# Kernel optimization log

Measured on AMD Instinct MI355X. Metric: run time of the kernel, lower is better.

The kernel has to match this reference:

```python
import jax, jax.numpy as jnp
import numpy as np

B, N, D_IN, D_OUT = 4, 2048, 1024, 1024

def setup_inputs() -> dict:
    key = jax.random.key(0)
    ks = jax.random.split(key, 7)
    s_in = 1.0 / np.sqrt(D_IN)
    return {
        "X": jax.random.normal(ks[0], (B, N, D_IN), dtype=jnp.float32),
        "Wq": jax.random.uniform(ks[1], (D_IN, D_OUT), jnp.float32, -s_in, s_in),
        "bq": jax.random.uniform(ks[2], (D_OUT,), jnp.float32, -s_in, s_in),
        "Wk": jax.random.uniform(ks[3], (D_IN, D_OUT), jnp.float32, -s_in, s_in),
        "bk": jax.random.uniform(ks[4], (D_OUT,), jnp.float32, -s_in, s_in),
        "Wv": jax.random.uniform(ks[5], (D_IN, D_OUT), jnp.float32, -s_in, s_in),
        "bv": jax.random.uniform(ks[6], (D_OUT,), jnp.float32, -s_in, s_in),
    }

def reference(X, Wq, bq, Wk, bk, Wv, bv):
    # QKV projections: [B,N,D_in] @ [D_in,D_out] -> [B,N,D_out]
    q = jnp.einsum('bnd,de->bne', X, Wq) + bq
    k = jnp.einsum('bnd,de->bne', X, Wk) + bk
    v = jnp.einsum('bnd,de->bne', X, Wv) + bv
    # Unscaled attention (faithful: original has no 1/sqrt(d))
    scores = jnp.einsum('bne,bme->bnm', q, k)  # [B,N,N]
    weights = jax.nn.softmax(scores, axis=-1)
    return jnp.einsum('bnm,bme->bne', weights, v)
```

## Files before the change

### kernel.cpp

```cpp
#include <hip/hip_runtime.h>
#include <hip/hip_bf16.h>
#include <hip/hip_fp16.h>
#include <stdint.h>
#include <math.h>


typedef unsigned short ushort_t;
typedef __attribute__((ext_vector_type(8))) _Float16  f16x8;
typedef __attribute__((ext_vector_type(4))) _Float16  f16x4;
typedef __attribute__((ext_vector_type(4))) float     f32x4;

__device__ __forceinline__ void async_load16(const void* g, void* l) {
  __builtin_amdgcn_global_load_lds(
      (const __attribute__((address_space(1))) void*)g,
      (__attribute__((address_space(3))) void*)l, 16, 0, 0);
}

__global__ __launch_bounds__(256)
void zv_gemm_kernel(const ushort_t* __restrict__ A, const ushort_t* __restrict__ BT,
                    const float* __restrict__ wkbq, const float* __restrict__ bvp,
                    __half* __restrict__ Zh, ushort_t* __restrict__ Vt)
{
  const int K = 1024;
  __shared__ ushort_t As[2][128 * 32];
  __shared__ ushort_t Bs[2][128 * 32];

  const int t    = threadIdx.x;
  const int lane = t & 63;
  const int wave = t >> 6;
  const int wm   = (wave >> 1) * 64;
  const int wn   = (wave & 1) * 64;

  const ushort_t* Ab = A + (long)blockIdx.y * 128 * K;
  const ushort_t* Bb = BT + (long)blockIdx.x * 128 * K;

  const int ldr = t >> 2;
  const int swzs = (ldr & 3) ^ ((ldr >> 2) & 3);
  const int ldc = ((t & 3) ^ swzs) * 8;
  const int frow = lane & 15;
  const int fsz  = (frow & 3) ^ ((frow >> 2) & 3);
  const int fo   = (((lane >> 4) ^ fsz)) * 8;

  f32x4 acc[4][4];
  const f32x4 zero = {0.0f, 0.0f, 0.0f, 0.0f};
#pragma unroll
  for (int i = 0; i < 4; ++i)
#pragma unroll
    for (int j = 0; j < 4; ++j) acc[i][j] = zero;

  for (int k0 = 0; k0 < K; k0 += 64) {
    __syncthreads();
    const ushort_t* ga = Ab + (long)ldr * K + k0 + ldc;
    const ushort_t* gb = Bb + (long)ldr * K + k0 + ldc;
#pragma unroll
    for (int h = 0; h < 2; ++h) {
      async_load16(ga + h * 32,                &As[h][t * 8]);
      async_load16(ga + h * 32 + 64 * (long)K, &As[h][2048 + t * 8]);
      async_load16(gb + h * 32,                &Bs[h][t * 8]);
      async_load16(gb + h * 32 + 64 * (long)K, &Bs[h][2048 + t * 8]);
    }
    __syncthreads();
#pragma unroll
    for (int h = 0; h < 2; ++h) {
      f16x8 af[4], bf[4];
#pragma unroll
      for (int i = 0; i < 4; ++i) {
        af[i] = *(const f16x8*)&As[h][(wm + i * 16 + frow) * 32 + fo];
        bf[i] = *(const f16x8*)&Bs[h][(wn + i * 16 + frow) * 32 + fo];
      }
#pragma unroll
      for (int mi = 0; mi < 4; ++mi)
#pragma unroll
        for (int ni = 0; ni < 4; ++ni)
          acc[mi][ni] = __builtin_amdgcn_mfma_f32_16x16x32_f16(af[mi], bf[ni], acc[mi][ni], 0, 0, 0);
    }
  }

  const int er = (lane >> 4) * 4;
  const int ec = lane & 15;
  const int tgt = blockIdx.x >> 3;
#pragma unroll
  for (int ni = 0; ni < 4; ++ni) {
    const int c = (blockIdx.x & 7) * 128 + wn + ni * 16 + ec;
    const float bval = (tgt == 0) ? wkbq[c] : bvp[c];
#pragma unroll
    for (int mi = 0; mi < 4; ++mi) {
      const long grow0 = (long)blockIdx.y * 128 + wm + mi * 16 + er;
      if (tgt == 0) {
#pragma unroll
        for (int r = 0; r < 4; ++r)
          Zh[(grow0 + r) * 1024 + c] = __float2half(acc[mi][ni][r] + bval);
      } else {
        const long b  = grow0 >> 11;
        const long ml = grow0 & 2047;
        f16x4 v4;
#pragma unroll
        for (int r = 0; r < 4; ++r) v4[r] = (_Float16)(acc[mi][ni][r] + bval);
        *(f16x4*)&Vt[b * 2097152 + (long)c * 2048 + ml] = v4;
      }
    }
  }
}

__global__ __launch_bounds__(256)
void gemm_f16_kernel(const ushort_t* __restrict__ A, const ushort_t* __restrict__ BT,
                     __half* __restrict__ C)
{
  const int K = 1024;
  __shared__ ushort_t As[2][128 * 32];
  __shared__ ushort_t Bs[2][128 * 32];

  const int t    = threadIdx.x;
  const int lane = t & 63;
  const int wave = t >> 6;
  const int wm   = (wave >> 1) * 64;
  const int wn   = (wave & 1) * 64;

  const ushort_t* Ab = A + (long)blockIdx.y * 128 * K;
  const ushort_t* Bb = BT + (long)blockIdx.x * 128 * K;

  const int ldr = t >> 2;
  const int swzs = (ldr & 3) ^ ((ldr >> 2) & 3);
  const int ldc = ((t & 3) ^ swzs) * 8;
  const int frow = lane & 15;
  const int fsz  = (frow & 3) ^ ((frow >> 2) & 3);
  const int fo   = (((lane >> 4) ^ fsz)) * 8;

  f32x4 acc[4][4];
  const f32x4 zero = {0.0f, 0.0f, 0.0f, 0.0f};
#pragma unroll
  for (int i = 0; i < 4; ++i)
#pragma unroll
    for (int j = 0; j < 4; ++j) acc[i][j] = zero;

  for (int k0 = 0; k0 < K; k0 += 64) {
    __syncthreads();
    const ushort_t* ga = Ab + (long)ldr * K + k0 + ldc;
    const ushort_t* gb = Bb + (long)ldr * K + k0 + ldc;
#pragma unroll
    for (int h = 0; h < 2; ++h) {
      async_load16(ga + h * 32,                &As[h][t * 8]);
      async_load16(ga + h * 32 + 64 * (long)K, &As[h][2048 + t * 8]);
      async_load16(gb + h * 32,                &Bs[h][t * 8]);
      async_load16(gb + h * 32 + 64 * (long)K, &Bs[h][2048 + t * 8]);
    }
    __syncthreads();
#pragma unroll
    for (int h = 0; h < 2; ++h) {
      f16x8 af[4], bf[4];
#pragma unroll
      for (int i = 0; i < 4; ++i) {
        af[i] = *(const f16x8*)&As[h][(wm + i * 16 + frow) * 32 + fo];
        bf[i] = *(const f16x8*)&Bs[h][(wn + i * 16 + frow) * 32 + fo];
      }
#pragma unroll
      for (int mi = 0; mi < 4; ++mi)
#pragma unroll
        for (int ni = 0; ni < 4; ++ni)
          acc[mi][ni] = __builtin_amdgcn_mfma_f32_16x16x32_f16(af[mi], bf[ni], acc[mi][ni], 0, 0, 0);
    }
  }

  const int er = (lane >> 4) * 4;
  const int ec = lane & 15;
#pragma unroll
  for (int ni = 0; ni < 4; ++ni) {
    const int gcol = blockIdx.x * 128 + wn + ni * 16 + ec;
#pragma unroll
    for (int mi = 0; mi < 4; ++mi)
#pragma unroll
      for (int r = 0; r < 4; ++r) {
        const long grow = (long)blockIdx.y * 128 + wm + mi * 16 + er + r;
        C[grow * 1024 + gcol] = __float2half(acc[mi][ni][r]);
      }
  }
}

__global__ __launch_bounds__(256)
void qk_gemm_kernel(const ushort_t* __restrict__ Z, const ushort_t* __restrict__ Xh,
                    __half* __restrict__ S, float* __restrict__ PM, float* __restrict__ PS)
{
  const int K = 1024;
  __shared__ ushort_t As[2][128 * 32];
  __shared__ ushort_t Bs[2][128 * 32];

  const int t    = threadIdx.x;
  const int lane = t & 63;
  const int wave = t >> 6;
  const int wm   = (wave >> 1) * 64;
  const int wn   = (wave & 1) * 64;
  const long z   = blockIdx.z;

  const ushort_t* Ab = Z + z * 2048 * 1024 + (long)blockIdx.y * 128 * K;
  const ushort_t* Bb = Xh + z * 2048 * 1024 + (long)blockIdx.x * 128 * K;
  __half* Sb = S + z * 2048 * 2048;

  const int ldr = t >> 2;
  const int swzs = (ldr & 3) ^ ((ldr >> 2) & 3);
  const int ldc = ((t & 3) ^ swzs) * 8;
  const int frow = lane & 15;
  const int fsz  = (frow & 3) ^ ((frow >> 2) & 3);
  const int fo   = (((lane >> 4) ^ fsz)) * 8;

  f32x4 acc[4][4];
  const f32x4 zero = {0.0f, 0.0f, 0.0f, 0.0f};
#pragma unroll
  for (int i = 0; i < 4; ++i)
#pragma unroll
    for (int j = 0; j < 4; ++j) acc[i][j] = zero;

  for (int k0 = 0; k0 < K; k0 += 64) {
    __syncthreads();
    const ushort_t* ga = Ab + (long)ldr * K + k0 + ldc;
    const ushort_t* gb = Bb + (long)ldr * K + k0 + ldc;
#pragma unroll
    for (int h = 0; h < 2; ++h) {
      async_load16(ga + h * 32,                &As[h][t * 8]);
      async_load16(ga + h * 32 + 64 * (long)K, &As[h][2048 + t * 8]);
      async_load16(gb + h * 32,                &Bs[h][t * 8]);
      async_load16(gb + h * 32 + 64 * (long)K, &Bs[h][2048 + t * 8]);
    }
    __syncthreads();
#pragma unroll
    for (int h = 0; h < 2; ++h) {
      f16x8 af[4], bf[4];
#pragma unroll
      for (int i = 0; i < 4; ++i) {
        af[i] = *(const f16x8*)&As[h][(wm + i * 16 + frow) * 32 + fo];
        bf[i] = *(const f16x8*)&Bs[h][(wn + i * 16 + frow) * 32 + fo];
      }
#pragma unroll
      for (int mi = 0; mi < 4; ++mi)
#pragma unroll
        for (int ni = 0; ni < 4; ++ni)
          acc[mi][ni] = __builtin_amdgcn_mfma_f32_16x16x32_f16(af[mi], bf[ni], acc[mi][ni], 0, 0, 0);
    }
  }

  const int er = (lane >> 4) * 4;
  const int ec = lane & 15;

  const int cc = blockIdx.x * 2 + (wave & 1);
  float* PMb = PM + z * 32 * 2048 + (long)cc * 2048;
  float* PSb = PS + z * 32 * 2048 + (long)cc * 2048;

#pragma unroll
  for (int mi = 0; mi < 4; ++mi)
#pragma unroll
    for (int r = 0; r < 4; ++r) {
      float m = fmaxf(fmaxf(acc[mi][0][r], acc[mi][1][r]),
                      fmaxf(acc[mi][2][r], acc[mi][3][r]));
      m = fmaxf(m, __shfl_xor(m, 1));
      m = fmaxf(m, __shfl_xor(m, 2));
      m = fmaxf(m, __shfl_xor(m, 4));
      m = fmaxf(m, __shfl_xor(m, 8));
      float s = 0.0f;
#pragma unroll
      for (int ni = 0; ni < 4; ++ni) {
        const float e = __expf(acc[mi][ni][r] - m);
        acc[mi][ni][r] = e;
        s += e;
      }
      s += __shfl_xor(s, 1);
      s += __shfl_xor(s, 2);
      s += __shfl_xor(s, 4);
      s += __shfl_xor(s, 8);
      if (ec == 0) {
        const long row = (long)blockIdx.y * 128 + wm + mi * 16 + er + r;
        PMb[row] = m;
        PSb[row] = s;
      }
    }

#pragma unroll
  for (int ni = 0; ni < 4; ++ni) {
    const long col = (long)blockIdx.x * 128 + wn + ni * 16 + ec;
#pragma unroll
    for (int mi = 0; mi < 4; ++mi)
#pragma unroll
      for (int r = 0; r < 4; ++r) {
        const long grow = (long)blockIdx.y * 128 + wm + mi * 16 + er + r;
        Sb[grow * 2048 + col] = __float2half(acc[mi][ni][r]);
      }
  }
}

__global__ __launch_bounds__(256)
void softmax_reduce_kernel(const float* __restrict__ PM, const float* __restrict__ PS,
                           float* __restrict__ Sc)
{
  const int r = blockIdx.x * 256 + threadIdx.x;
  const int b = r >> 11, row = r & 2047;
  const long base = (long)b * 32 * 2048 + row;
  float m = -3.4e38f;
#pragma unroll
  for (int cb = 0; cb < 32; ++cb) m = fmaxf(m, PM[base + cb * 2048]);
  float l = 0.0f;
#pragma unroll
  for (int cb = 0; cb < 32; ++cb) l += PS[base + cb * 2048] * __expf(PM[base + cb * 2048] - m);
  const float inv = 1.0f / l;
#pragma unroll
  for (int cb = 0; cb < 32; ++cb) Sc[base + cb * 2048] = __expf(PM[base + cb * 2048] - m) * inv;
}

__global__ __launch_bounds__(256)
void pv_gemm_kernel(const ushort_t* __restrict__ S, const ushort_t* __restrict__ Vt,
                    const float* __restrict__ Sc, float* __restrict__ Out)
{
  const int K = 2048;
  __shared__ ushort_t As[2][128 * 32];
  __shared__ ushort_t Bs[2][128 * 32];

  const int t    = threadIdx.x;
  const int lane = t & 63;
  const int wave = t >> 6;
  const int wm   = (wave >> 1) * 64;
  const int wn   = (wave & 1) * 64;
  const long z   = blockIdx.z;

  const ushort_t* Ab = S + z * 2048 * 2048 + (long)blockIdx.y * 128 * K;
  const ushort_t* Bb = Vt + z * 1024 * 2048 + (long)blockIdx.x * 128 * K;
  const float* Scb = Sc + z * 32 * 2048;
  float* Cb = Out + z * 2048 * 1024;

  const int ldr = t >> 2;
  const int swzs = (ldr & 3) ^ ((ldr >> 2) & 3);
  const int ldc = ((t & 3) ^ swzs) * 8;
  const int frow = lane & 15;
  const int fsz  = (frow & 3) ^ ((frow >> 2) & 3);
  const int fo   = (((lane >> 4) ^ fsz)) * 8;

  const int arow0 = blockIdx.y * 128 + wm + frow;

  f32x4 acc[4][4];
  const f32x4 zero = {0.0f, 0.0f, 0.0f, 0.0f};
#pragma unroll
  for (int i = 0; i < 4; ++i)
#pragma unroll
    for (int j = 0; j < 4; ++j) acc[i][j] = zero;

  for (int k0 = 0; k0 < K; k0 += 64) {
    const int cb = k0 >> 6;
    _Float16 sc16[4];
#pragma unroll
    for (int i = 0; i < 4; ++i)
      sc16[i] = (_Float16)Scb[(long)cb * 2048 + arow0 + i * 16];

    __syncthreads();
    const ushort_t* ga = Ab + (long)ldr * K + k0 + ldc;
    const ushort_t* gb = Bb + (long)ldr * K + k0 + ldc;
#pragma unroll
    for (int h = 0; h < 2; ++h) {
      async_load16(ga + h * 32,                &As[h][t * 8]);
      async_load16(ga + h * 32 + 64 * (long)K, &As[h][2048 + t * 8]);
      async_load16(gb + h * 32,                &Bs[h][t * 8]);
      async_load16(gb + h * 32 + 64 * (long)K, &Bs[h][2048 + t * 8]);
    }
    __syncthreads();
#pragma unroll
    for (int h = 0; h < 2; ++h) {
      f16x8 af[4], bf[4];
#pragma unroll
      for (int i = 0; i < 4; ++i) {
        af[i] = *(const f16x8*)&As[h][(wm + i * 16 + frow) * 32 + fo] * sc16[i];
        bf[i] = *(const f16x8*)&Bs[h][(wn + i * 16 + frow) * 32 + fo];
      }
#pragma unroll
      for (int mi = 0; mi < 4; ++mi)
#pragma unroll
        for (int ni = 0; ni < 4; ++ni)
          acc[mi][ni] = __builtin_amdgcn_mfma_f32_16x16x32_f16(af[mi], bf[ni], acc[mi][ni], 0, 0, 0);
    }
  }

  const int er = (lane >> 4) * 4;
  const int ec = lane & 15;
#pragma unroll
  for (int ni = 0; ni < 4; ++ni) {
    const int gcol = blockIdx.x * 128 + wn + ni * 16 + ec;
#pragma unroll
    for (int mi = 0; mi < 4; ++mi) {
#pragma unroll
      for (int r = 0; r < 4; ++r) {
        const long grow = (long)blockIdx.y * 128 + wm + mi * 16 + er + r;
        Cb[grow * 1024 + gcol] = acc[mi][ni][r];
      }
    }
  }
}

__global__ __launch_bounds__(256)
void prep_kernel(const float* __restrict__ X, __half* __restrict__ Xh, int nx,
                 const float* __restrict__ Wq, __half* __restrict__ Wqh,
                 const float* __restrict__ Wk, __half* __restrict__ Wkh,
                 const float* __restrict__ Wv, __half* __restrict__ Wvt)
{
  const int bid = blockIdx.x;
  const int tid = threadIdx.x;
  if (bid < nx + 1024) {
    const float* src; __half* dst; long base;
    if (bid < nx)          { src = X;  dst = Xh;  base = (long)bid * 2048; }
    else if (bid < nx+512) { src = Wq; dst = Wqh; base = (long)(bid - nx) * 2048; }
    else                   { src = Wk; dst = Wkh; base = (long)(bid - nx - 512) * 2048; }
    const long i = base + (long)tid * 8;
    const float4 a = *(const float4*)(src + i);
    const float4 b = *(const float4*)(src + i + 4);
    f16x8 h;
    h[0] = (_Float16)a.x; h[1] = (_Float16)a.y; h[2] = (_Float16)a.z; h[3] = (_Float16)a.w;
    h[4] = (_Float16)b.x; h[5] = (_Float16)b.y; h[6] = (_Float16)b.z; h[7] = (_Float16)b.w;
    *(f16x8*)((ushort_t*)dst + i) = h;
  } else {
    __shared__ float tile[32][33];
    const int t2 = bid - (nx + 1024);
    const int c0 = (t2 & 31) * 32;
    const int r0 = (t2 >> 5) * 32;
    const int tx = tid & 31;
    const int ty = tid >> 5;
#pragma unroll
    for (int i = 0; i < 32; i += 8)
      tile[ty + i][tx] = Wv[(long)(r0 + ty + i) * 1024 + (c0 + tx)];
    __syncthreads();
#pragma unroll
    for (int i = 0; i < 32; i += 8)
      Wvt[(long)(c0 + ty + i) * 1024 + (r0 + tx)] = __float2half(tile[tx][ty + i]);
  }
}

__global__ __launch_bounds__(256)
void cvt_f32_f16_kernel(const float* __restrict__ src, __half* __restrict__ dst, long n)
{
  const long i = ((long)blockIdx.x * 256 + threadIdx.x) * 8;
  if (i + 8 > n) return;
  const float4 a = *(const float4*)(src + i);
  const float4 b = *(const float4*)(src + i + 4);
  f16x8 h;
  h[0] = (_Float16)a.x; h[1] = (_Float16)a.y; h[2] = (_Float16)a.z; h[3] = (_Float16)a.w;
  h[4] = (_Float16)b.x; h[5] = (_Float16)b.y; h[6] = (_Float16)b.z; h[7] = (_Float16)b.w;
  *(f16x8*)((ushort_t*)dst + i) = h;
}

__global__ __launch_bounds__(256)
void wkbq_kernel(const float* __restrict__ Wk, const float* __restrict__ bq,
                 float* __restrict__ wkbq)
{
  const int wave = threadIdx.x >> 6, lane = threadIdx.x & 63;
  const int d = blockIdx.x * 4 + wave;
  const float* row = Wk + (long)d * 1024;
  float acc = 0.0f;
#pragma unroll
  for (int p = 0; p < 4; ++p) {
    const int e = p * 256 + lane * 4;
    const float4 wv = *(const float4*)(row + e);
    const float4 bv = *(const float4*)(bq + e);
    acc += wv.x * bv.x + wv.y * bv.y + wv.z * bv.z + wv.w * bv.w;
  }
#pragma unroll
  for (int off = 32; off > 0; off >>= 1) acc += __shfl_xor(acc, off, 64);
  if (lane == 0) wkbq[d] = acc;
}

extern "C" void kernel_launch(void* const* d_in, const int* in_sizes, int n_in,
                              void* d_out, int out_size, void* d_ws, size_t ws_size,
                              hipStream_t stream)
{
  const int  Bb = 4, Nn = 2048, Dd = 1024;
  const long BN = (long)Bb * Nn;

  const float* X  = (const float*)d_in[0];
  const float* Wq = (const float*)d_in[1];
  const float* bq = (const float*)d_in[2];
  const float* Wk = (const float*)d_in[3];
  const float* bk = (const float*)d_in[4];  (void)bk;
  const float* Wv = (const float*)d_in[5];
  const float* bv = (const float*)d_in[6];
  float* Out      = (float*)d_out;

  uint8_t* w = (uint8_t*)d_ws;
  ushort_t* Wqh   = (ushort_t*)w;  w += (size_t)Dd * Dd * 2;
  ushort_t* Wkh   = (ushort_t*)w;  w += (size_t)Dd * Dd * 2;
  ushort_t* MtWvt = (ushort_t*)w;  w += (size_t)2 * Dd * Dd * 2;
  ushort_t* Mt  = MtWvt;
  ushort_t* Wvt = MtWvt + (size_t)Dd * Dd;
  float* wkbq = (float*)w;  w += (size_t)Dd * 4;

  const size_t statsBytes = (size_t)Bb * 32 * Nn * 4;
  const size_t fullNeed = (size_t)8 * Dd * Dd * 2 + Dd * 4
                        + 3 * ((size_t)BN * Dd * 2)
                        + (size_t)Bb * Nn * Nn * 2
                        + 3 * statsBytes;

  wkbq_kernel<<<dim3(Dd / 4), 256, 0, stream>>>(Wk, bq, wkbq);

  if (ws_size >= fullNeed) {
    ushort_t* Xh = (ushort_t*)w;  w += (size_t)BN * Dd * 2;
    ushort_t* Zh = (ushort_t*)w;  w += (size_t)BN * Dd * 2;
    ushort_t* Vt = (ushort_t*)w;  w += (size_t)BN * Dd * 2;
    ushort_t* S  = (ushort_t*)w;  w += (size_t)Bb * Nn * Nn * 2;
    float*    PM = (float*)w;     w += statsBytes;
    float*    PS = (float*)w;     w += statsBytes;
    float*    Sc = (float*)w;

    const int nx = (int)(BN * Dd / 2048);
    prep_kernel<<<dim3(nx + 2048), 256, 0, stream>>>(
        X, (__half*)Xh, nx, Wq, (__half*)Wqh, Wk, (__half*)Wkh, Wv, (__half*)Wvt);

    gemm_f16_kernel<<<dim3(Dd / 128, Dd / 128), 256, 0, stream>>>(Wkh, Wqh, (__half*)Mt);

    zv_gemm_kernel<<<dim3(2 * Dd / 128, BN / 128), 256, 0, stream>>>(
        Xh, MtWvt, wkbq, bv, (__half*)Zh, Vt);

    qk_gemm_kernel<<<dim3(Nn / 128, Nn / 128, Bb), 256, 0, stream>>>(
        Zh, Xh, (__half*)S, PM, PS);

    softmax_reduce_kernel<<<dim3((unsigned)(Bb * Nn / 256)), 256, 0, stream>>>(PM, PS, Sc);

    pv_gemm_kernel<<<dim3(Dd / 128, Nn / 128, Bb), 256, 0, stream>>>(S, Vt, Sc, Out);
  } else {
    ushort_t* Xh = (ushort_t*)w;  w += (size_t)Nn * Dd * 2;
    ushort_t* Zh = (ushort_t*)w;  w += (size_t)Nn * Dd * 2;
    ushort_t* Vt = (ushort_t*)w;  w += (size_t)Nn * Dd * 2;
    ushort_t* S  = (ushort_t*)w;  w += (size_t)Nn * Nn * 2;
    float*    PM = (float*)w;     w += (size_t)32 * Nn * 4;
    float*    PS = (float*)w;     w += (size_t)32 * Nn * 4;
    float*    Sc = (float*)w;

    prep_kernel<<<dim3(2048), 256, 0, stream>>>(
        nullptr, nullptr, 0, Wq, (__half*)Wqh, Wk, (__half*)Wkh, Wv, (__half*)Wvt);
    gemm_f16_kernel<<<dim3(Dd / 128, Dd / 128), 256, 0, stream>>>(Wkh, Wqh, (__half*)Mt);

    for (int b = 0; b < Bb; ++b) {
      const float* Xb = X + (long)b * Nn * Dd;
      cvt_f32_f16_kernel<<<dim3((unsigned)((long)Nn * Dd / (8 * 256))), 256, 0, stream>>>(
          Xb, (__half*)Xh, (long)Nn * Dd);
      zv_gemm_kernel<<<dim3(2 * Dd / 128, Nn / 128), 256, 0, stream>>>(
          Xh, MtWvt, wkbq, bv, (__half*)Zh, Vt);
      qk_gemm_kernel<<<dim3(Nn / 128, Nn / 128, 1), 256, 0, stream>>>(
          Zh, Xh, (__half*)S, PM, PS);
      softmax_reduce_kernel<<<dim3(Nn / 256), 256, 0, stream>>>(PM, PS, Sc);
      pv_gemm_kernel<<<dim3(Dd / 128, Nn / 128, 1), 256, 0, stream>>>(
          S, Vt, Sc, Out + (long)b * Nn * Dd);
    }
  }
}
```

Baseline: 285.8 us.

## Fuse Wk·Wqᵀ GEMM, bias fold and weight conversion into one prep kernel

The separate wkbq kernel, the Wq/Wk fp16 conversion pass and the Wk·Wq^T GEMM are merged into the prep kernel as heterogeneous block ranges. The GEMM blocks now read fp32 weights directly and convert them in registers before writing to LDS, so the Wqh/Wkh intermediates and their workspace disappear. This removes two kernel launches and one round trip of the fp16 weight copies. In exchange the 64 GEMM blocks use synchronous loads instead of async LDS loads, and the larger shared-memory footprint applies to every block in the launch, which may reduce occupancy for the conversion blocks.

```diff
diff --git a/kernel.cpp b/kernel.cpp
--- a/kernel.cpp
+++ b/kernel.cpp
@@ -99,80 +99,6 @@
         *(f16x4*)&Vt[b * 2097152 + (long)c * 2048 + ml] = v4;
       }
     }
-  }
-}
-
-__global__ __launch_bounds__(256)
-void gemm_f16_kernel(const ushort_t* __restrict__ A, const ushort_t* __restrict__ BT,
-                     __half* __restrict__ C)
-{
-  const int K = 1024;
-  __shared__ ushort_t As[2][128 * 32];
-  __shared__ ushort_t Bs[2][128 * 32];
-
-  const int t    = threadIdx.x;
-  const int lane = t & 63;
-  const int wave = t >> 6;
-  const int wm   = (wave >> 1) * 64;
-  const int wn   = (wave & 1) * 64;
-
-  const ushort_t* Ab = A + (long)blockIdx.y * 128 * K;
-  const ushort_t* Bb = BT + (long)blockIdx.x * 128 * K;
-
-  const int ldr = t >> 2;
-  const int swzs = (ldr & 3) ^ ((ldr >> 2) & 3);
-  const int ldc = ((t & 3) ^ swzs) * 8;
-  const int frow = lane & 15;
-  const int fsz  = (frow & 3) ^ ((frow >> 2) & 3);
-  const int fo   = (((lane >> 4) ^ fsz)) * 8;
-
-  f32x4 acc[4][4];
-  const f32x4 zero = {0.0f, 0.0f, 0.0f, 0.0f};
-#pragma unroll
-  for (int i = 0; i < 4; ++i)
-#pragma unroll
-    for (int j = 0; j < 4; ++j) acc[i][j] = zero;
-
-  for (int k0 = 0; k0 < K; k0 += 64) {
-    __syncthreads();
-    const ushort_t* ga = Ab + (long)ldr * K + k0 + ldc;
-    const ushort_t* gb = Bb + (long)ldr * K + k0 + ldc;
-#pragma unroll
-    for (int h = 0; h < 2; ++h) {
-      async_load16(ga + h * 32,                &As[h][t * 8]);
-      async_load16(ga + h * 32 + 64 * (long)K, &As[h][2048 + t * 8]);
-      async_load16(gb + h * 32,                &Bs[h][t * 8]);
-      async_load16(gb + h * 32 + 64 * (long)K, &Bs[h][2048 + t * 8]);
-    }
-    __syncthreads();
-#pragma unroll
-    for (int h = 0; h < 2; ++h) {
-      f16x8 af[4], bf[4];
-#pragma unroll
-      for (int i = 0; i < 4; ++i) {
-        af[i] = *(const f16x8*)&As[h][(wm + i * 16 + frow) * 32 + fo];
-        bf[i] = *(const f16x8*)&Bs[h][(wn + i * 16 + frow) * 32 + fo];
-      }
-#pragma unroll
-      for (int mi = 0; mi < 4; ++mi)
-#pragma unroll
-        for (int ni = 0; ni < 4; ++ni)
-          acc[mi][ni] = __builtin_amdgcn_mfma_f32_16x16x32_f16(af[mi], bf[ni], acc[mi][ni], 0, 0, 0);
-    }
-  }
-
-  const int er = (lane >> 4) * 4;
-  const int ec = lane & 15;
-#pragma unroll
-  for (int ni = 0; ni < 4; ++ni) {
-    const int gcol = blockIdx.x * 128 + wn + ni * 16 + ec;
-#pragma unroll
-    for (int mi = 0; mi < 4; ++mi)
-#pragma unroll
-      for (int r = 0; r < 4; ++r) {
-        const long grow = (long)blockIdx.y * 128 + wm + mi * 16 + er + r;
-        C[grow * 1024 + gcol] = __float2half(acc[mi][ni][r]);
-      }
   }
 }
 
@@ -391,27 +317,107 @@
 
 __global__ __launch_bounds__(256)
 void prep_kernel(const float* __restrict__ X, __half* __restrict__ Xh, int nx,
-                 const float* __restrict__ Wq, __half* __restrict__ Wqh,
-                 const float* __restrict__ Wk, __half* __restrict__ Wkh,
-                 const float* __restrict__ Wv, __half* __restrict__ Wvt)
-{
+                 const float* __restrict__ Wq, const float* __restrict__ Wk,
+                 const float* __restrict__ Wv, __half* __restrict__ Wvt,
+                 const float* __restrict__ bq, float* __restrict__ wkbq,
+                 __half* __restrict__ Mt)
+{
+  __shared__ ushort_t As[2][128 * 32];
+  __shared__ ushort_t Bs[2][128 * 32];
+  __shared__ float tile[32][33];
+
   const int bid = blockIdx.x;
   const int tid = threadIdx.x;
-  if (bid < nx + 1024) {
-    const float* src; __half* dst; long base;
-    if (bid < nx)          { src = X;  dst = Xh;  base = (long)bid * 2048; }
-    else if (bid < nx+512) { src = Wq; dst = Wqh; base = (long)(bid - nx) * 2048; }
-    else                   { src = Wk; dst = Wkh; base = (long)(bid - nx - 512) * 2048; }
-    const long i = base + (long)tid * 8;
-    const float4 a = *(const float4*)(src + i);
-    const float4 b = *(const float4*)(src + i + 4);
-    f16x8 h;
-    h[0] = (_Float16)a.x; h[1] = (_Float16)a.y; h[2] = (_Float16)a.z; h[3] = (_Float16)a.w;
-    h[4] = (_Float16)b.x; h[5] = (_Float16)b.y; h[6] = (_Float16)b.z; h[7] = (_Float16)b.w;
-    *(f16x8*)((ushort_t*)dst + i) = h;
-  } else {
-    __shared__ float tile[32][33];
-    const int t2 = bid - (nx + 1024);
+
+  if (bid < 64) {
+    const int bx = bid & 7, by = bid >> 3;
+    const int lane = tid & 63, wave = tid >> 6;
+    const int wm = (wave >> 1) * 64, wn = (wave & 1) * 64;
+    const int ldr = tid >> 2;
+    const int swzs = (ldr & 3) ^ ((ldr >> 2) & 3);
+    const int ldc = ((tid & 3) ^ swzs) * 8;
+    const int frow = lane & 15;
+    const int fsz  = (frow & 3) ^ ((frow >> 2) & 3);
+    const int fo   = (((lane >> 4) ^ fsz)) * 8;
+
+    const float* Ar = Wk + (long)(by * 128 + ldr) * 1024;
+    const float* Br = Wq + (long)(bx * 128 + ldr) * 1024;
+
+    f32x4 acc[4][4];
+    const f32x4 zero = {0.0f, 0.0f, 0.0f, 0.0f};
+#pragma unroll
+    for (int i = 0; i < 4; ++i)
+#pragma unroll
+      for (int j = 0; j < 4; ++j) acc[i][j] = zero;
+
+    for (int k0 = 0; k0 < 1024; k0 += 64) {
+      __syncthreads();
+#pragma unroll
+      for (int h = 0; h < 2; ++h) {
+        const int kc = k0 + h * 32 + ldc;
+#pragma unroll
+        for (int half = 0; half < 2; ++half) {
+          const long roff = (long)half * 64 * 1024;
+          const float4 a0 = *(const float4*)(Ar + roff + kc);
+          const float4 a1 = *(const float4*)(Ar + roff + kc + 4);
+          const float4 b0 = *(const float4*)(Br + roff + kc);
+          const float4 b1 = *(const float4*)(Br + roff + kc + 4);
+          f16x8 ah, bh;
+          ah[0]=(_Float16)a0.x; ah[1]=(_Float16)a0.y; ah[2]=(_Float16)a0.z; ah[3]=(_Float16)a0.w;
+          ah[4]=(_Float16)a1.x; ah[5]=(_Float16)a1.y; ah[6]=(_Float16)a1.z; ah[7]=(_Float16)a1.w;
+          bh[0]=(_Float16)b0.x; bh[1]=(_Float16)b0.y; bh[2]=(_Float16)b0.z; bh[3]=(_Float16)b0.w;
+          bh[4]=(_Float16)b1.x; bh[5]=(_Float16)b1.y; bh[6]=(_Float16)b1.z; bh[7]=(_Float16)b1.w;
+          *(f16x8*)&As[h][half * 2048 + tid * 8] = ah;
+          *(f16x8*)&Bs[h][half * 2048 + tid * 8] = bh;
+        }
+      }
+      __syncthreads();
+#pragma unroll
+      for (int h = 0; h < 2; ++h) {
+        f16x8 af[4], bf[4];
+#pragma unroll
+        for (int i = 0; i < 4; ++i) {
+          af[i] = *(const f16x8*)&As[h][(wm + i * 16 + frow) * 32 + fo];
+          bf[i] = *(const f16x8*)&Bs[h][(wn + i * 16 + frow) * 32 + fo];
+        }
+#pragma unroll
+        for (int mi = 0; mi < 4; ++mi)
+#pragma unroll
+          for (int ni = 0; ni < 4; ++ni)
+            acc[mi][ni] = __builtin_amdgcn_mfma_f32_16x16x32_f16(af[mi], bf[ni], acc[mi][ni], 0, 0, 0);
+      }
+    }
+
+    const int er = (lane >> 4) * 4;
+    const int ec = lane & 15;
+#pragma unroll
+    for (int ni = 0; ni < 4; ++ni) {
+      const int gcol = bx * 128 + wn + ni * 16 + ec;
+#pragma unroll
+      for (int mi = 0; mi < 4; ++mi)
+#pragma unroll
+        for (int r = 0; r < 4; ++r) {
+          const long grow = (long)by * 128 + wm + mi * 16 + er + r;
+          Mt[grow * 1024 + gcol] = __float2half(acc[mi][ni][r]);
+        }
+    }
+  } else if (bid < 320) {
+    const int wave = tid >> 6, lane = tid & 63;
+    const int d = (bid - 64) * 4 + wave;
+    const float* row = Wk + (long)d * 1024;
+    float acc = 0.0f;
+#pragma unroll
+    for (int p = 0; p < 4; ++p) {
+      const int e = p * 256 + lane * 4;
+      const float4 wv = *(const float4*)(row + e);
+      const float4 bv = *(const float4*)(bq + e);
+      acc += wv.x * bv.x + wv.y * bv.y + wv.z * bv.z + wv.w * bv.w;
+    }
+#pragma unroll
+    for (int off = 32; off > 0; off >>= 1) acc += __shfl_xor(acc, off, 64);
+    if (lane == 0) wkbq[d] = acc;
+  } else if (bid < 1344) {
+    const int t2 = bid - 320;
     const int c0 = (t2 & 31) * 32;
     const int r0 = (t2 >> 5) * 32;
     const int tx = tid & 31;
@@ -423,6 +429,14 @@
 #pragma unroll
     for (int i = 0; i < 32; i += 8)
       Wvt[(long)(c0 + ty + i) * 1024 + (r0 + tx)] = __float2half(tile[tx][ty + i]);
+  } else {
+    const long i = (long)(bid - 1344) * 2048 + (long)tid * 8;
+    const float4 a = *(const float4*)(X + i);
+    const float4 b = *(const float4*)(X + i + 4);
+    f16x8 h;
+    h[0]=(_Float16)a.x; h[1]=(_Float16)a.y; h[2]=(_Float16)a.z; h[3]=(_Float16)a.w;
+    h[4]=(_Float16)b.x; h[5]=(_Float16)b.y; h[6]=(_Float16)b.z; h[7]=(_Float16)b.w;
+    *(f16x8*)((ushort_t*)Xh + i) = h;
   }
 }
 
@@ -439,26 +453,6 @@
   *(f16x8*)((ushort_t*)dst + i) = h;
 }
 
-__global__ __launch_bounds__(256)
-void wkbq_kernel(const float* __restrict__ Wk, const float* __restrict__ bq,
-                 float* __restrict__ wkbq)
-{
-  const int wave = threadIdx.x >> 6, lane = threadIdx.x & 63;
-  const int d = blockIdx.x * 4 + wave;
-  const float* row = Wk + (long)d * 1024;
-  float acc = 0.0f;
-#pragma unroll
-  for (int p = 0; p < 4; ++p) {
-    const int e = p * 256 + lane * 4;
-    const float4 wv = *(const float4*)(row + e);
-    const float4 bv = *(const float4*)(bq + e);
-    acc += wv.x * bv.x + wv.y * bv.y + wv.z * bv.z + wv.w * bv.w;
-  }
-#pragma unroll
-  for (int off = 32; off > 0; off >>= 1) acc += __shfl_xor(acc, off, 64);
-  if (lane == 0) wkbq[d] = acc;
-}
-
 extern "C" void kernel_launch(void* const* d_in, const int* in_sizes, int n_in,
                               void* d_out, int out_size, void* d_ws, size_t ws_size,
                               hipStream_t stream)
@@ -476,20 +470,16 @@
   float* Out      = (float*)d_out;
 
   uint8_t* w = (uint8_t*)d_ws;
-  ushort_t* Wqh   = (ushort_t*)w;  w += (size_t)Dd * Dd * 2;
-  ushort_t* Wkh   = (ushort_t*)w;  w += (size_t)Dd * Dd * 2;
   ushort_t* MtWvt = (ushort_t*)w;  w += (size_t)2 * Dd * Dd * 2;
   ushort_t* Mt  = MtWvt;
   ushort_t* Wvt = MtWvt + (size_t)Dd * Dd;
   float* wkbq = (float*)w;  w += (size_t)Dd * 4;
 
   const size_t statsBytes = (size_t)Bb * 32 * Nn * 4;
-  const size_t fullNeed = (size_t)8 * Dd * Dd * 2 + Dd * 4
+  const size_t fullNeed = (size_t)4 * Dd * Dd * 2 + Dd * 4
                         + 3 * ((size_t)BN * Dd * 2)
                         + (size_t)Bb * Nn * Nn * 2
                         + 3 * statsBytes;
-
-  wkbq_kernel<<<dim3(Dd / 4), 256, 0, stream>>>(Wk, bq, wkbq);
 
   if (ws_size >= fullNeed) {
     ushort_t* Xh = (ushort_t*)w;  w += (size_t)BN * Dd * 2;
@@ -501,10 +491,8 @@
     float*    Sc = (float*)w;
 
     const int nx = (int)(BN * Dd / 2048);
-    prep_kernel<<<dim3(nx + 2048), 256, 0, stream>>>(
-        X, (__half*)Xh, nx, Wq, (__half*)Wqh, Wk, (__half*)Wkh, Wv, (__half*)Wvt);
-
-    gemm_f16_kernel<<<dim3(Dd / 128, Dd / 128), 256, 0, stream>>>(Wkh, Wqh, (__half*)Mt);
+    prep_kernel<<<dim3(1344 + nx), 256, 0, stream>>>(
+        X, (__half*)Xh, nx, Wq, Wk, Wv, (__half*)Wvt, bq, wkbq, (__half*)Mt);
 
     zv_gemm_kernel<<<dim3(2 * Dd / 128, BN / 128), 256, 0, stream>>>(
         Xh, MtWvt, wkbq, bv, (__half*)Zh, Vt);
@@ -524,9 +512,8 @@
     float*    PS = (float*)w;     w += (size_t)32 * Nn * 4;
     float*    Sc = (float*)w;
 
-    prep_kernel<<<dim3(2048), 256, 0, stream>>>(
-        nullptr, nullptr, 0, Wq, (__half*)Wqh, Wk, (__half*)Wkh, Wv, (__half*)Wvt);
-    gemm_f16_kernel<<<dim3(Dd / 128, Dd / 128), 256, 0, stream>>>(Wkh, Wqh, (__half*)Mt);
+    prep_kernel<<<dim3(1344), 256, 0, stream>>>(
+        nullptr, nullptr, 0, Wq, Wk, Wv, (__half*)Wvt, bq, wkbq, (__half*)Mt);
 
     for (int b = 0; b < Bb; ++b) {
       const float* Xb = X + (long)b * Nn * Dd;
```

Result: no change. 283.9 us (-0.7%).
